# Kernel tuning notes

Measured on AMD Instinct MI355X. Metric: run time of the kernel, lower is better.

## Reference

```python
import jax, jax.numpy as jnp
import numpy as np
import math

B, T, C = 2, 2048, 2048
H, KV, HD = 16, 4, 128          # n_head, n_kv_head, head_dim
REP = H // KV
FFN = 5632                      # multiple_of-rounded 2/3 * 4 * n_embd
EPS = 1e-5


def setup_inputs() -> dict:
    key = jax.random.key(0)
    ks = jax.random.split(key, 10)
    s = 0.02
    x = jax.random.normal(ks[0], (B, T, C), dtype=jnp.float32)
    # RoPE table: (T, HD/2, 2) = (cos, sin)
    inv_freq = 1.0 / (10000.0 ** (np.arange(0, HD, 2, dtype=np.float32) / HD))
    ang = np.arange(T, dtype=np.float32)[:, None] * inv_freq[None, :]
    freqs_cis = jnp.asarray(np.stack([np.cos(ang), np.sin(ang)], axis=-1))
    wq = s * jax.random.normal(ks[1], (H * HD, C), dtype=jnp.float32)
    wk = s * jax.random.normal(ks[2], (KV * HD, C), dtype=jnp.float32)
    wv = s * jax.random.normal(ks[3], (KV * HD, C), dtype=jnp.float32)
    wo = s * jax.random.normal(ks[4], (C, H * HD), dtype=jnp.float32)
    w1 = s * jax.random.normal(ks[5], (FFN, C), dtype=jnp.float32)
    w2 = s * jax.random.normal(ks[6], (FFN, C), dtype=jnp.float32)
    c_proj = s * jax.random.normal(ks[7], (C, FFN), dtype=jnp.float32)
    g1 = jnp.ones((C,), dtype=jnp.float32)
    g2 = jnp.ones((C,), dtype=jnp.float32)
    return {"x": x, "freqs_cis": freqs_cis, "wq": wq, "wk": wk, "wv": wv,
            "wo": wo, "w1": w1, "w2": w2, "c_proj": c_proj, "g1": g1, "g2": g2}


def _rmsnorm(x, g, eps=EPS):
    return x * jax.lax.rsqrt(jnp.mean(x * x, axis=-1, keepdims=True) + eps) * g


def _rope(t, freqs_cis):
    # t: (B, T, nH, HD); freqs_cis: (T, HD/2, 2)
    tr = t.reshape(*t.shape[:-1], HD // 2, 2)
    cos = freqs_cis[None, :, None, :, 0]
    sin = freqs_cis[None, :, None, :, 1]
    out = jnp.stack([tr[..., 0] * cos - tr[..., 1] * sin,
                     tr[..., 0] * sin + tr[..., 1] * cos], axis=-1)
    return out.reshape(t.shape)


def reference(x, freqs_cis, wq, wk, wv, wo, w1, w2, c_proj, g1, g2):
    h = _rmsnorm(x, g1)
    q = (h @ wq.T).reshape(B, T, H, HD)
    k = (h @ wk.T).reshape(B, T, KV, HD)
    v = (h @ wv.T).reshape(B, T, KV, HD)
    q = _rope(q, freqs_cis)
    k = _rope(k, freqs_cis)
    # GQA: group query heads by kv head; never materialize expanded K/V
    q = q.transpose(0, 2, 1, 3).reshape(B, KV, REP, T, HD)  # b g r q d
    k = k.transpose(0, 2, 1, 3)                              # b g k d
    v = v.transpose(0, 2, 1, 3)                              # b g k d
    scale = 1.0 / math.sqrt(HD)
    scores = jnp.einsum('bgrqd,bgkd->bgrqk', q, k) * scale
    causal = jnp.tril(jnp.ones((T, T), dtype=bool))
    scores = jnp.where(causal, scores, jnp.float32(-1e30))
    attn = jax.nn.softmax(scores, axis=-1)
    y = jnp.einsum('bgrqk,bgkd->bgrqd', attn, v)
    y = y.reshape(B, H, T, HD).transpose(0, 2, 1, 3).reshape(B, T, C)
    x = x + y @ wo.T
    h2 = _rmsnorm(x, g2)
    mlp = (jax.nn.silu(h2 @ w1.T) * (h2 @ w2.T)) @ c_proj.T
    return x + mlp
```

## Files before the change

kernel.cpp:

```cpp
#include <hip/hip_runtime.h>
#include <hip/hip_bf16.h>
#include <math.h>

#define TT   2048
#define CC   2048
#define NB   2
#define NH   16
#define NKV  4
#define HDIM 128
#define NFFN 5632

typedef __attribute__((ext_vector_type(8))) short     bf8;
typedef __attribute__((ext_vector_type(4))) float     f32x4;
typedef __attribute__((ext_vector_type(8))) unsigned short u16x8;
typedef __attribute__((ext_vector_type(4))) unsigned short u16x4;

__device__ __forceinline__ float b2f(unsigned short u) {
    union { unsigned u; float f; } v; v.u = ((unsigned)u) << 16; return v.f;
}
__device__ __forceinline__ unsigned short f2bf(float f) {
    union { float f; unsigned u; } v; v.f = f;
    unsigned r = (v.u + 0x7fffu + ((v.u >> 16) & 1u)) >> 16;
    return (unsigned short)r;
}
__device__ __forceinline__ void gll16(const void* g, void* l) {
    __builtin_amdgcn_global_load_lds((const __attribute__((address_space(1))) void*)g,
                                     (__attribute__((address_space(3))) void*)l, 16, 0, 0);
}

__global__ __launch_bounds__(256) void cvt_k(const float* __restrict__ in,
        __hip_bfloat16* __restrict__ out)
{
    const size_t i = ((size_t)blockIdx.x * 256 + threadIdx.x) * 8;
    float4 a = *(const float4*)(in + i);
    float4 b = *(const float4*)(in + i + 4);
    u16x8 v;
    v[0] = f2bf(a.x); v[1] = f2bf(a.y); v[2] = f2bf(a.z); v[3] = f2bf(a.w);
    v[4] = f2bf(b.x); v[5] = f2bf(b.y); v[6] = f2bf(b.z); v[7] = f2bf(b.w);
    *(u16x8*)((unsigned short*)out + i) = v;
}

__global__ __launch_bounds__(256) void rms_f32_k(const float* __restrict__ x,
        const float* __restrict__ g, __hip_bfloat16* __restrict__ o)
{
    const size_t row = blockIdx.x;
    const int e0 = threadIdx.x * 8;
    float4 a = *(const float4*)(x + row * CC + e0);
    float4 b = *(const float4*)(x + row * CC + e0 + 4);
    float vals[8] = {a.x, a.y, a.z, a.w, b.x, b.y, b.z, b.w};
    float s = 0.f;
    #pragma unroll
    for (int e = 0; e < 8; ++e) s += vals[e] * vals[e];
    #pragma unroll
    for (int off = 32; off; off >>= 1) s += __shfl_xor(s, off);
    __shared__ float wsum[4];
    if ((threadIdx.x & 63) == 0) wsum[threadIdx.x >> 6] = s;
    __syncthreads();
    float scale = rsqrtf((wsum[0] + wsum[1] + wsum[2] + wsum[3]) * (1.0f / CC) + 1e-5f);
    float4 g0 = *(const float4*)(g + e0);
    float4 g1 = *(const float4*)(g + e0 + 4);
    float gs[8] = {g0.x, g0.y, g0.z, g0.w, g1.x, g1.y, g1.z, g1.w};
    u16x8 ov;
    #pragma unroll
    for (int e = 0; e < 8; ++e) ov[e] = f2bf(vals[e] * scale * gs[e]);
    *(u16x8*)((unsigned short*)o + row * CC + e0) = ov;
}

__global__ __launch_bounds__(256) void rms_bf16_k(const __hip_bfloat16* __restrict__ x,
        const float* __restrict__ g, __hip_bfloat16* __restrict__ o)
{
    const size_t row = blockIdx.x;
    const int e0 = threadIdx.x * 8;
    u16x8 xv = *(const u16x8*)((const unsigned short*)x + row * CC + e0);
    float vals[8];
    #pragma unroll
    for (int e = 0; e < 8; ++e) vals[e] = b2f(xv[e]);
    float s = 0.f;
    #pragma unroll
    for (int e = 0; e < 8; ++e) s += vals[e] * vals[e];
    #pragma unroll
    for (int off = 32; off; off >>= 1) s += __shfl_xor(s, off);
    __shared__ float wsum[4];
    if ((threadIdx.x & 63) == 0) wsum[threadIdx.x >> 6] = s;
    __syncthreads();
    float scale = rsqrtf((wsum[0] + wsum[1] + wsum[2] + wsum[3]) * (1.0f / CC) + 1e-5f);
    float4 g0 = *(const float4*)(g + e0);
    float4 g1 = *(const float4*)(g + e0 + 4);
    float gs[8] = {g0.x, g0.y, g0.z, g0.w, g1.x, g1.y, g1.z, g1.w};
    u16x8 ov;
    #pragma unroll
    for (int e = 0; e < 8; ++e) ov[e] = f2bf(vals[e] * scale * gs[e]);
    *(u16x8*)((unsigned short*)o + row * CC + e0) = ov;
}

__global__ __launch_bounds__(256) void rope_k(__hip_bfloat16* __restrict__ t,
        const float* __restrict__ fc, int nh)
{
    const int e = blockIdx.x * 256 + threadIdx.x;
    const int per_row = nh * 64;
    const int row = e / per_row;
    const int rem = e - row * per_row;
    const int hh = rem >> 6, i = rem & 63;
    const int tt = row & (TT - 1);
    const float c = fc[tt * HDIM + i * 2];
    const float s = fc[tt * HDIM + i * 2 + 1];
    unsigned short* p = (unsigned short*)t + (size_t)row * (nh * HDIM) + hh * HDIM + i * 2;
    float a = b2f(p[0]), b = b2f(p[1]);
    p[0] = f2bf(a * c - b * s);
    p[1] = f2bf(a * s + b * c);
}

#define GBM 128
#define GBN 128
#define GBK 32

template<int EPI, int OUTB>
__global__ __launch_bounds__(256) void gemm_db(
        const __hip_bfloat16* __restrict__ A,
        const __hip_bfloat16* __restrict__ W,
        const void* __restrict__ Rp,
        void* __restrict__ Cp,
        int M, int N, int K)
{
    __shared__ alignas(16) __hip_bfloat16 As[2][GBM][GBK];
    __shared__ alignas(16) __hip_bfloat16 Ws[2][GBN][GBK];
    const int tid  = threadIdx.x;
    const int lane = tid & 63;
    const int wid  = tid >> 6;
    const int wr = wid >> 1, wc = wid & 1;
    const int nwg = gridDim.x * gridDim.y;
    const int lin = blockIdx.y * gridDim.x + blockIdx.x;
    const int nlin = (lin & 7) * (nwg >> 3) + (lin >> 3);
    const int bxs = nlin % gridDim.x, bys = nlin / gridDim.x;
    const int bm = bys * GBM, bn = bxs * GBN;
    const int l4  = lane >> 2;
    const int lk8 = (lane & 3) * 8;
    const int fr  = lane & 15;
    const int fk  = (lane >> 4) * 8;

    f32x4 acc[4][4];
    #pragma unroll
    for (int m = 0; m < 4; ++m)
        #pragma unroll
        for (int n = 0; n < 4; ++n) acc[m][n] = (f32x4){0.f, 0.f, 0.f, 0.f};

    const __hip_bfloat16* ga0 = A + (size_t)(bm + wid * 32 + l4) * K + lk8;
    const __hip_bfloat16* ga1 = A + (size_t)(bm + wid * 32 + 16 + l4) * K + lk8;
    const __hip_bfloat16* gw0 = W + (size_t)(bn + wid * 32 + l4) * K + lk8;
    const __hip_bfloat16* gw1 = W + (size_t)(bn + wid * 32 + 16 + l4) * K + lk8;

    const int nt = K >> 5;
    gll16(ga0, &As[0][wid * 32][0]);
    gll16(ga1, &As[0][wid * 32 + 16][0]);
    gll16(gw0, &Ws[0][wid * 32][0]);
    gll16(gw1, &Ws[0][wid * 32 + 16][0]);

    #pragma unroll 2
    for (int t = 0; t < nt; ++t) {
        const int cur = t & 1;
        __syncthreads();
        if (t + 1 < nt) {
            const int k1 = (t + 1) << 5;
            const int nx = cur ^ 1;
            gll16(ga0 + k1, &As[nx][wid * 32][0]);
            gll16(ga1 + k1, &As[nx][wid * 32 + 16][0]);
            gll16(gw0 + k1, &Ws[nx][wid * 32][0]);
            gll16(gw1 + k1, &Ws[nx][wid * 32 + 16][0]);
        }
        bf8 af[4];
        #pragma unroll
        for (int m = 0; m < 4; ++m)
            af[m] = *(const bf8*)&As[cur][wr * 64 + m * 16 + fr][fk];
        #pragma unroll
        for (int n = 0; n < 4; ++n) {
            bf8 wf = *(const bf8*)&Ws[cur][wc * 64 + n * 16 + fr][fk];
            #pragma unroll
            for (int m = 0; m < 4; ++m)
                acc[m][n] = __builtin_amdgcn_mfma_f32_16x16x32_bf16(af[m], wf, acc[m][n], 0, 0, 0);
        }
    }

    const int rj = (lane >> 4) * 4;
    #pragma unroll
    for (int m = 0; m < 4; ++m) {
        #pragma unroll
        for (int j = 0; j < 4; ++j) {
            const size_t row = (size_t)(bm + wr * 64 + m * 16 + rj + j);
            #pragma unroll
            for (int n = 0; n < 4; ++n) {
                const size_t col = (size_t)(bn + wc * 64 + n * 16 + fr);
                float v = acc[m][n][j];
                if (EPI == 1) v += ((const float*)Rp)[row * N + col];
                if (EPI == 2) v += b2f(((const unsigned short*)Rp)[row * N + col]);
                if (EPI == 3) {
                    float gv = b2f(((const unsigned short*)Rp)[row * N + col]);
                    v = (gv / (1.0f + __expf(-gv))) * v;
                }
                if (OUTB) ((unsigned short*)Cp)[row * N + col] = f2bf(v);
                else      ((float*)Cp)[row * N + col] = v;
            }
        }
    }
}

__global__ __launch_bounds__(256) void gemm_qkv_db(
        const __hip_bfloat16* __restrict__ A,
        const __hip_bfloat16* __restrict__ W,
        __hip_bfloat16* __restrict__ qo,
        __hip_bfloat16* __restrict__ ko,
        __hip_bfloat16* __restrict__ vto,
        int M, int K)
{
    __shared__ alignas(16) __hip_bfloat16 As[2][GBM][GBK];
    __shared__ alignas(16) __hip_bfloat16 Ws[2][GBN][GBK];
    const int tid  = threadIdx.x;
    const int lane = tid & 63;
    const int wid  = tid >> 6;
    const int wr = wid >> 1, wc = wid & 1;
    const int nwg = gridDim.x * gridDim.y;
    const int lin = blockIdx.y * gridDim.x + blockIdx.x;
    const int nlin = (lin & 7) * (nwg >> 3) + (lin >> 3);
    const int bxs = nlin % gridDim.x, bys = nlin / gridDim.x;
    const int bm = bys * GBM, bn = bxs * GBN;
    const int l4  = lane >> 2;
    const int lk8 = (lane & 3) * 8;
    const int fr  = lane & 15;
    const int fk  = (lane >> 4) * 8;

    f32x4 acc[4][4];
    #pragma unroll
    for (int m = 0; m < 4; ++m)
        #pragma unroll
        for (int n = 0; n < 4; ++n) acc[m][n] = (f32x4){0.f, 0.f, 0.f, 0.f};

    const __hip_bfloat16* ga0 = A + (size_t)(bm + wid * 32 + l4) * K + lk8;
    const __hip_bfloat16* ga1 = A + (size_t)(bm + wid * 32 + 16 + l4) * K + lk8;
    const __hip_bfloat16* gw0 = W + (size_t)(bn + wid * 32 + l4) * K + lk8;
    const __hip_bfloat16* gw1 = W + (size_t)(bn + wid * 32 + 16 + l4) * K + lk8;

    const int nt = K >> 5;
    gll16(ga0, &As[0][wid * 32][0]);
    gll16(ga1, &As[0][wid * 32 + 16][0]);
    gll16(gw0, &Ws[0][wid * 32][0]);
    gll16(gw1, &Ws[0][wid * 32 + 16][0]);

    #pragma unroll 2
    for (int t = 0; t < nt; ++t) {
        const int cur = t & 1;
        __syncthreads();
        if (t + 1 < nt) {
            const int k1 = (t + 1) << 5;
            const int nx = cur ^ 1;
            gll16(ga0 + k1, &As[nx][wid * 32][0]);
            gll16(ga1 + k1, &As[nx][wid * 32 + 16][0]);
            gll16(gw0 + k1, &Ws[nx][wid * 32][0]);
            gll16(gw1 + k1, &Ws[nx][wid * 32 + 16][0]);
        }
        bf8 af[4];
        #pragma unroll
        for (int m = 0; m < 4; ++m)
            af[m] = *(const bf8*)&As[cur][wr * 64 + m * 16 + fr][fk];
        #pragma unroll
        for (int n = 0; n < 4; ++n) {
            bf8 wf = *(const bf8*)&Ws[cur][wc * 64 + n * 16 + fr][fk];
            #pragma unroll
            for (int m = 0; m < 4; ++m)
                acc[m][n] = __builtin_amdgcn_mfma_f32_16x16x32_bf16(af[m], wf, acc[m][n], 0, 0, 0);
        }
    }

    const int rj = (lane >> 4) * 4;
    #pragma unroll
    for (int m = 0; m < 4; ++m) {
        #pragma unroll
        for (int n = 0; n < 4; ++n) {
            const int col = bn + wc * 64 + n * 16 + fr;
            const int row0 = bm + wr * 64 + m * 16 + rj;
            if (col < 2048) {
                #pragma unroll
                for (int j = 0; j < 4; ++j)
                    ((unsigned short*)qo)[(size_t)(row0 + j) * CC + col] = f2bf(acc[m][n][j]);
            } else if (col < 2560) {
                #pragma unroll
                for (int j = 0; j < 4; ++j)
                    ((unsigned short*)ko)[(size_t)(row0 + j) * (NKV * HDIM) + (col - 2048)] = f2bf(acc[m][n][j]);
            } else {
                const int vc = col - 2560;
                const int g = vc >> 7, d = vc & 127;
                const int b = row0 >> 11, t0 = row0 & (TT - 1);
                unsigned short* vp = (unsigned short*)vto +
                    ((size_t)(b * NKV + g) * HDIM + d) * TT + t0;
                u16x4 ov;
                #pragma unroll
                for (int j = 0; j < 4; ++j) ov[j] = f2bf(acc[m][n][j]);
                *(u16x4*)vp = ov;
            }
        }
    }
}

#define AQB 128
#define AKV 64

__global__ __launch_bounds__(512) void attn_mfma(const __hip_bfloat16* __restrict__ q,
        const __hip_bfloat16* __restrict__ k, const __hip_bfloat16* __restrict__ vt,
        __hip_bfloat16* __restrict__ y)
{
    __shared__ alignas(16) unsigned short Ks[AKV * HDIM];
    __shared__ alignas(16) unsigned short Vs[HDIM * AKV];
    __shared__ alignas(16) unsigned short Ps[AQB * AKV];

    const int qt = (TT / AQB - 1) - blockIdx.x;
    const int h  = blockIdx.y;
    const int b  = blockIdx.z;
    const int g  = h >> 2;
    const int qbase = qt * AQB;

    const int tid  = threadIdx.x;
    const int lane = tid & 63;
    const int wid  = tid >> 6;
    const int fr   = lane & 15;
    const int fk8  = (lane >> 4) * 8;
    const int rj   = (lane >> 4) * 4;

    bf8 qf[4];
    {
        const unsigned short* qp = (const unsigned short*)q +
            (size_t)(b * TT + qbase + wid * 16 + fr) * CC + h * HDIM;
        #pragma unroll
        for (int c = 0; c < 4; ++c)
            qf[c] = *(const bf8*)(qp + c * 32 + fk8);
    }
    const unsigned short* vtb = (const unsigned short*)vt + (size_t)(b * NKV + g) * HDIM * TT;

    f32x4 oacc[8];
    float m_r[4], l_r[4];
    #pragma unroll
    for (int n = 0; n < 8; ++n) oacc[n] = (f32x4){0.f, 0.f, 0.f, 0.f};
    #pragma unroll
    for (int j = 0; j < 4; ++j) { m_r[j] = -1e30f; l_r[j] = 0.f; }

    const float scale = 0.08838834764831845f;
    const int ntiles = qbase / AKV + 2;
    const int kjr = tid >> 3;
    const int kkc = (tid & 7) * 16;
    const int vdr = tid >> 2;
    const int vjc = (tid & 3) * 16;

    for (int tile = 0; tile < ntiles; ++tile) {
        const int jbase = tile * AKV;
        __syncthreads();
        {
            const unsigned short* kp = (const unsigned short*)k +
                ((size_t)(b * TT + jbase + kjr) * (NKV * HDIM)) + g * HDIM + kkc;
            const unsigned short* vp = vtb + (size_t)vdr * TT + jbase + vjc;
            #pragma unroll
            for (int c = 0; c < 2; ++c) {
                u16x8 kv = *(const u16x8*)(kp + c * 8);
                const int byteK = (kjr * 256 + (kkc + c * 8) * 2) ^ ((kjr & 7) << 4);
                *(u16x8*)((char*)Ks + byteK) = kv;
                u16x8 vv = *(const u16x8*)(vp + c * 8);
                const int byteV = (vdr * 128 + (vjc + c * 8) * 2) ^ ((vdr & 7) << 4);
                *(u16x8*)((char*)Vs + byteV) = vv;
            }
        }
        __syncthreads();

        f32x4 s[4];
        #pragma unroll
        for (int n = 0; n < 4; ++n) s[n] = (f32x4){0.f, 0.f, 0.f, 0.f};
        __builtin_amdgcn_s_setprio(1);
        #pragma unroll
        for (int c = 0; c < 4; ++c) {
            #pragma unroll
            for (int n = 0; n < 4; ++n) {
                const int j = n * 16 + fr;
                const int byteB = (j * 256 + (c * 32 + fk8) * 2) ^ ((j & 7) << 4);
                bf8 kf = *(const bf8*)((char*)Ks + byteB);
                s[n] = __builtin_amdgcn_mfma_f32_16x16x32_bf16(qf[c], kf, s[n], 0, 0, 0);
            }
        }
        __builtin_amdgcn_s_setprio(0);

        #pragma unroll
        for (int jj = 0; jj < 4; ++jj) {
            const int qg = qbase + wid * 16 + rj + jj;
            float sv[4];
            #pragma unroll
            for (int n = 0; n < 4; ++n) {
                const int jg = jbase + n * 16 + fr;
                sv[n] = (jg <= qg) ? s[n][jj] * scale : -1e30f;
            }
            float tmax = fmaxf(fmaxf(sv[0], sv[1]), fmaxf(sv[2], sv[3]));
            tmax = fmaxf(tmax, __shfl_xor(tmax, 1));
            tmax = fmaxf(tmax, __shfl_xor(tmax, 2));
            tmax = fmaxf(tmax, __shfl_xor(tmax, 4));
            tmax = fmaxf(tmax, __shfl_xor(tmax, 8));
            const float mnew = fmaxf(m_r[jj], tmax);
            const float alpha = __expf(m_r[jj] - mnew);
            m_r[jj] = mnew;
            const int prow = wid * 16 + rj + jj;
            float tsum = 0.f;
            #pragma unroll
            for (int n = 0; n < 4; ++n) {
                const float p = __expf(sv[n] - mnew);
                tsum += p;
                const int byteP = (prow * 128 + (n * 16 + fr) * 2) ^ ((prow & 7) << 4);
                *(unsigned short*)((char*)Ps + byteP) = f2bf(p);
            }
            tsum += __shfl_xor(tsum, 1);
            tsum += __shfl_xor(tsum, 2);
            tsum += __shfl_xor(tsum, 4);
            tsum += __shfl_xor(tsum, 8);
            l_r[jj] = l_r[jj] * alpha + tsum;
            #pragma unroll
            for (int n = 0; n < 8; ++n) oacc[n][jj] *= alpha;
        }

        __builtin_amdgcn_s_setprio(1);
        #pragma unroll
        for (int c2 = 0; c2 < 2; ++c2) {
            const int prow = wid * 16 + fr;
            const int byteA = (prow * 128 + (c2 * 32 + fk8) * 2) ^ ((prow & 7) << 4);
            bf8 pf = *(const bf8*)((char*)Ps + byteA);
            #pragma unroll
            for (int n = 0; n < 8; ++n) {
                const int d = n * 16 + fr;
                const int byteB = (d * 128 + (c2 * 32 + fk8) * 2) ^ ((d & 7) << 4);
                bf8 vf = *(const bf8*)((char*)Vs + byteB);
                oacc[n] = __builtin_amdgcn_mfma_f32_16x16x32_bf16(pf, vf, oacc[n], 0, 0, 0);
            }
        }
        __builtin_amdgcn_s_setprio(0);
    }

    #pragma unroll
    for (int jj = 0; jj < 4; ++jj) {
        const float inv = 1.0f / l_r[jj];
        unsigned short* yrow = (unsigned short*)y +
            ((size_t)(b * TT + qbase + wid * 16 + rj + jj) * CC) + h * HDIM;
        #pragma unroll
        for (int n = 0; n < 8; ++n)
            yrow[n * 16 + fr] = f2bf(oacc[n][jj] * inv);
    }
}

extern "C" void kernel_launch(void* const* d_in, const int* in_sizes, int n_in,
                              void* d_out, int out_size, void* d_ws, size_t ws_size,
                              hipStream_t stream)
{
    (void)in_sizes; (void)n_in; (void)out_size; (void)ws_size;
    const float* x     = (const float*)d_in[0];
    const float* fc    = (const float*)d_in[1];
    const float* wq    = (const float*)d_in[2];
    const float* wk    = (const float*)d_in[3];
    const float* wv    = (const float*)d_in[4];
    const float* wo    = (const float*)d_in[5];
    const float* w1    = (const float*)d_in[6];
    const float* w2    = (const float*)d_in[7];
    const float* cproj = (const float*)d_in[8];
    const float* g1    = (const float*)d_in[9];
    const float* g2    = (const float*)d_in[10];
    float* out = (float*)d_out;

    const int ROWS = NB * TT;
    unsigned char* wsb = (unsigned char*)d_ws;
    __hip_bfloat16* x2b = (__hip_bfloat16*)(wsb);
    __hip_bfloat16* hb  = (__hip_bfloat16*)(wsb + 16777216u);
    __hip_bfloat16* w1b = (__hip_bfloat16*)(wsb + 33554432u);
    __hip_bfloat16* w2b = (__hip_bfloat16*)(wsb + 56623104u);
    __hip_bfloat16* G1  = (__hip_bfloat16*)(wsb + 79691776u);
    __hip_bfloat16* cpb = w1b;
    __hip_bfloat16* qb   = (__hip_bfloat16*)(wsb + 33554432u);
    __hip_bfloat16* kb   = (__hip_bfloat16*)(wsb + 50331648u);
    __hip_bfloat16* vtb  = (__hip_bfloat16*)(wsb + 54525952u);
    __hip_bfloat16* yb   = (__hip_bfloat16*)(wsb + 58720256u);
    __hip_bfloat16* wbuf = (__hip_bfloat16*)(wsb + 75497472u);

    rms_f32_k<<<ROWS, 256, 0, stream>>>(x, g1, hb);
    cvt_k<<<(CC * CC) / 2048, 256, 0, stream>>>(wq, wbuf);
    cvt_k<<<(NKV * HDIM * CC) / 2048, 256, 0, stream>>>(wk, wbuf + (size_t)2048 * CC);
    cvt_k<<<(NKV * HDIM * CC) / 2048, 256, 0, stream>>>(wv, wbuf + (size_t)2560 * CC);
    gemm_qkv_db<<<dim3(3072 / GBN, ROWS / GBM), 256, 0, stream>>>(hb, wbuf, qb, kb, vtb, ROWS, CC);
    rope_k<<<(ROWS * NH * 64) / 256, 256, 0, stream>>>(qb, fc, NH);
    rope_k<<<(ROWS * NKV * 64) / 256, 256, 0, stream>>>(kb, fc, NKV);
    attn_mfma<<<dim3(TT / AQB, NH, NB), 512, 0, stream>>>(qb, kb, vtb, yb);
    cvt_k<<<(CC * CC) / 2048, 256, 0, stream>>>(wo, wbuf);
    gemm_db<1, 1><<<dim3(CC / GBN, ROWS / GBM), 256, 0, stream>>>(yb, wbuf, x, x2b, ROWS, CC, CC);
    rms_bf16_k<<<ROWS, 256, 0, stream>>>(x2b, g2, hb);
    cvt_k<<<(NFFN * CC) / 2048, 256, 0, stream>>>(w1, w1b);
    cvt_k<<<(NFFN * CC) / 2048, 256, 0, stream>>>(w2, w2b);
    gemm_db<0, 1><<<dim3(NFFN / GBN, ROWS / GBM), 256, 0, stream>>>(hb, w1b, nullptr, G1, ROWS, NFFN, CC);
    gemm_db<3, 1><<<dim3(NFFN / GBN, ROWS / GBM), 256, 0, stream>>>(hb, w2b, G1, G1, ROWS, NFFN, CC);
    cvt_k<<<(CC * NFFN) / 2048, 256, 0, stream>>>(cproj, cpb);
    gemm_db<2, 0><<<dim3(CC / GBN, ROWS / GBM), 256, 0, stream>>>(G1, cpb, x2b, out, ROWS, CC, NFFN);
}
```

Baseline: 725.1 us.

## Add 8-wave 128x256 MFMA GEMM with ping-pong scheduling for MLP GEMMs

Adds a new 512-thread GEMM kernel that uses a 128x256x64 tile, double-buffered direct global-to-LDS loads with an XOR swizzle, an XCD-aware block remap, and barrier/setprio interleaving of the MFMA and LDS-read phases. It replaces the existing double-buffered GEMM for the three MLP matmuls (w1, w2 with SiLU gate, c_proj with residual). The aim is higher MFMA utilisation and better operand reuse on the largest GEMMs. In exchange the larger tile reduces grid size (NFFN/256 = 22 columns) and the many barriers can stall waves. The epilogue still writes scalar, uncoalesced stores.

```diff
diff --git a/kernel.cpp b/kernel.cpp
--- a/kernel.cpp
+++ b/kernel.cpp
@@ -299,6 +299,137 @@
     }
 }
 
+#define PBM 128
+#define PBN 256
+#define PBK 64
+
+template<int EPI, int OUTB>
+__global__ __launch_bounds__(512) void gemm_8p(
+        const __hip_bfloat16* __restrict__ A,
+        const __hip_bfloat16* __restrict__ W,
+        const void* __restrict__ Rp,
+        void* __restrict__ Cp,
+        int M, int N, int K)
+{
+    __shared__ alignas(16) __hip_bfloat16 As[2][PBM][PBK];
+    __shared__ alignas(16) __hip_bfloat16 Ws[2][PBN][PBK];
+    const int tid  = threadIdx.x;
+    const int lane = tid & 63;
+    const int wid  = tid >> 6;
+    const int wr = wid >> 2, wc = wid & 3;
+    const int nwg = gridDim.x * gridDim.y;
+    const int lin = blockIdx.y * gridDim.x + blockIdx.x;
+    const int nlin = (lin & 7) * (nwg >> 3) + (lin >> 3);
+    const int bxs = nlin % gridDim.x, bys = nlin / gridDim.x;
+    const int bm = bys * PBM, bn = bxs * PBN;
+    const int fr = lane & 15;
+    const int hi = lane >> 4;
+
+    f32x4 acc[4][4];
+    #pragma unroll
+    for (int m = 0; m < 4; ++m)
+        #pragma unroll
+        for (int n = 0; n < 4; ++n) acc[m][n] = (f32x4){0.f, 0.f, 0.f, 0.f};
+
+    const unsigned short* Ag = (const unsigned short*)A;
+    const unsigned short* Wg = (const unsigned short*)W;
+
+    auto STAGE = [&](int buf, int k0) {
+        #pragma unroll
+        for (int l = 0; l < 2; ++l) {
+            const int s = l * 512 + tid;
+            const int row = s >> 3;
+            const int srcb = ((s & 7) * 16) ^ ((row & 7) << 4);
+            gll16(Ag + (size_t)(bm + row) * K + k0 + (srcb >> 1),
+                  (unsigned short*)&As[buf][0][0] + (l * 512 + wid * 64) * 8);
+        }
+        #pragma unroll
+        for (int l = 0; l < 4; ++l) {
+            const int s = l * 512 + tid;
+            const int row = s >> 3;
+            const int srcb = ((s & 7) * 16) ^ ((row & 7) << 4);
+            gll16(Wg + (size_t)(bn + row) * K + k0 + (srcb >> 1),
+                  (unsigned short*)&Ws[buf][0][0] + (l * 512 + wid * 64) * 8);
+        }
+    };
+
+    const int nt = K >> 6;
+    STAGE(0, 0);
+    __syncthreads();
+
+    for (int t = 0; t < nt; ++t) {
+        const int cur = t & 1;
+        const char* Ab = (const char*)&As[cur][0][0];
+        const char* Bb = (const char*)&Ws[cur][0][0];
+
+        bf8 bF[4][2];
+        #pragma unroll
+        for (int n = 0; n < 4; ++n) {
+            const int row = wc * 64 + n * 16 + fr;
+            #pragma unroll
+            for (int kk = 0; kk < 2; ++kk) {
+                const int off = (kk * 64 + hi * 16) ^ ((row & 7) << 4);
+                bF[n][kk] = *(const bf8*)(Bb + row * 128 + off);
+            }
+        }
+        bf8 a0, a1;
+        {
+            const int row = wr * 64 + fr;
+            a0 = *(const bf8*)(Ab + row * 128 + ((hi * 16)      ^ ((row & 7) << 4)));
+            a1 = *(const bf8*)(Ab + row * 128 + ((64 + hi * 16) ^ ((row & 7) << 4)));
+        }
+        if (t + 1 < nt) STAGE(cur ^ 1, (t + 1) * PBK);
+        __builtin_amdgcn_s_barrier();
+        __builtin_amdgcn_s_setprio(1);
+        #pragma unroll
+        for (int n = 0; n < 4; ++n) {
+            acc[0][n] = __builtin_amdgcn_mfma_f32_16x16x32_bf16(a0, bF[n][0], acc[0][n], 0, 0, 0);
+            acc[0][n] = __builtin_amdgcn_mfma_f32_16x16x32_bf16(a1, bF[n][1], acc[0][n], 0, 0, 0);
+        }
+        __builtin_amdgcn_s_setprio(0);
+        __builtin_amdgcn_s_barrier();
+
+        #pragma unroll
+        for (int m = 1; m < 4; ++m) {
+            const int row = wr * 64 + m * 16 + fr;
+            bf8 am0 = *(const bf8*)(Ab + row * 128 + ((hi * 16)      ^ ((row & 7) << 4)));
+            bf8 am1 = *(const bf8*)(Ab + row * 128 + ((64 + hi * 16) ^ ((row & 7) << 4)));
+            __builtin_amdgcn_s_barrier();
+            __builtin_amdgcn_s_setprio(1);
+            #pragma unroll
+            for (int n = 0; n < 4; ++n) {
+                acc[m][n] = __builtin_amdgcn_mfma_f32_16x16x32_bf16(am0, bF[n][0], acc[m][n], 0, 0, 0);
+                acc[m][n] = __builtin_amdgcn_mfma_f32_16x16x32_bf16(am1, bF[n][1], acc[m][n], 0, 0, 0);
+            }
+            __builtin_amdgcn_s_setprio(0);
+            if (m < 3) __builtin_amdgcn_s_barrier();
+        }
+        __syncthreads();
+    }
+
+    const int rj = hi * 4;
+    #pragma unroll
+    for (int m = 0; m < 4; ++m) {
+        #pragma unroll
+        for (int j = 0; j < 4; ++j) {
+            const size_t row = (size_t)(bm + wr * 64 + m * 16 + rj + j);
+            #pragma unroll
+            for (int n = 0; n < 4; ++n) {
+                const size_t col = (size_t)(bn + wc * 64 + n * 16 + fr);
+                float v = acc[m][n][j];
+                if (EPI == 1) v += ((const float*)Rp)[row * N + col];
+                if (EPI == 2) v += b2f(((const unsigned short*)Rp)[row * N + col]);
+                if (EPI == 3) {
+                    float gv = b2f(((const unsigned short*)Rp)[row * N + col]);
+                    v = (gv / (1.0f + __expf(-gv))) * v;
+                }
+                if (OUTB) ((unsigned short*)Cp)[row * N + col] = f2bf(v);
+                else      ((float*)Cp)[row * N + col] = v;
+            }
+        }
+    }
+}
+
 #define AQB 128
 #define AKV 64
 
@@ -490,8 +621,8 @@
     rms_bf16_k<<<ROWS, 256, 0, stream>>>(x2b, g2, hb);
     cvt_k<<<(NFFN * CC) / 2048, 256, 0, stream>>>(w1, w1b);
     cvt_k<<<(NFFN * CC) / 2048, 256, 0, stream>>>(w2, w2b);
-    gemm_db<0, 1><<<dim3(NFFN / GBN, ROWS / GBM), 256, 0, stream>>>(hb, w1b, nullptr, G1, ROWS, NFFN, CC);
-    gemm_db<3, 1><<<dim3(NFFN / GBN, ROWS / GBM), 256, 0, stream>>>(hb, w2b, G1, G1, ROWS, NFFN, CC);
+    gemm_8p<0, 1><<<dim3(NFFN / PBN, ROWS / PBM), 512, 0, stream>>>(hb, w1b, nullptr, G1, ROWS, NFFN, CC);
+    gemm_8p<3, 1><<<dim3(NFFN / PBN, ROWS / PBM), 512, 0, stream>>>(hb, w2b, G1, G1, ROWS, NFFN, CC);
     cvt_k<<<(CC * NFFN) / 2048, 256, 0, stream>>>(cproj, cpb);
-    gemm_db<2, 0><<<dim3(CC / GBN, ROWS / GBM), 256, 0, stream>>>(G1, cpb, x2b, out, ROWS, CC, NFFN);
-}
+    gemm_8p<2, 0><<<dim3(CC / PBN, ROWS / PBM), 512, 0, stream>>>(G1, cpb, x2b, out, ROWS, CC, NFFN);
+}
```

Result: faster. 686.2 us (-5.4%).
